# Kernel optimization log

Measured on AMD Instinct MI355X. Metric: run time of the kernel, lower is better.

## Reference

```python
import jax, jax.numpy as jnp
import numpy as np

# Neighbor offsets (di, dj) such that shifted[i, j] = x[i + di, j + dj],
# matching the original ZeroPad2d+slice construction for gates 1..8:
# (left-top, center-top, right-top, left-center, right-center,
#  left-bottom, center-bottom, right-bottom)
OFFSETS = ((1, 1), (1, 0), (1, -1), (0, 1), (0, -1), (-1, 1), (-1, 0), (-1, -1))
PROP_TIME = 4


def _shift(x, di, dj):
    """Zero-padded spatial shift over the last two dims: out[i,j] = x[i+di, j+dj]."""
    xp = jnp.pad(x, [(0, 0)] * (x.ndim - 2) + [(1, 1), (1, 1)])
    H, W = x.shape[-2], x.shape[-1]
    return xp[..., 1 + di:1 + di + H, 1 + dj:1 + dj + W]


def setup_inputs() -> dict:
    key = jax.random.key(0)
    k1, k2 = jax.random.split(key)
    guidance = jax.random.normal(k1, (16, 8, 512, 512), dtype=jnp.float32)
    blur_depth = jax.random.normal(k2, (16, 1, 512, 512), dtype=jnp.float32)
    return {"guidance": guidance, "blur_depth": blur_depth}


def reference(guidance, blur_depth):
    # guidance: [B, 8, H, W]; blur_depth: [B, C=1, H, W]
    # Shifted gates: equivalent to pad-by-offset then slice [1:-1, 1:-1].
    gate_wb = jnp.stack(
        [_shift(guidance[:, k], di, dj) for k, (di, dj) in enumerate(OFFSETS)],
        axis=1,
    )  # [B, 8, H, W]
    abs_weight = jnp.sum(jnp.abs(gate_wb), axis=1, keepdims=True)  # [B, 1, H, W]
    gate_wb = gate_wb / abs_weight
    gate_sum = jnp.sum(gate_wb, axis=1)  # [B, H, W]

    raw = blur_depth
    result = blur_depth  # [B, C, H, W]
    for _ in range(PROP_TIME):
        shifted = jnp.stack(
            [_shift(result, di, dj) for (di, dj) in OFFSETS], axis=1
        )  # [B, 8, C, H, W]
        # gate_wb broadcast over channel dim C (gate_wb[:, :, None] -> [B,8,1,H,W])
        result = jnp.sum(gate_wb[:, :, None] * shifted, axis=1)  # [B, C, H, W]
        result = (1.0 - gate_sum)[:, None] * raw + result
    return result
```

## Files before the change

### kernel.cpp

```cpp
#include <hip/hip_runtime.h>


#define TILE 32
#define G    40
#define GM   38
#define NTHREADS 512

__launch_bounds__(NTHREADS)
__global__ void affprop_kernel(const float* __restrict__ guidance,
                               const float* __restrict__ blur,
                               float* __restrict__ out) {
    __shared__ float sGate[8][GM * GM];
    __shared__ float sBase[GM * GM];
    __shared__ float sA[G * G];
    __shared__ float sB[G * G];

    const int tid = threadIdx.x;
    const int bx0 = blockIdx.x * TILE;
    const int by0 = blockIdx.y * TILE;
    const int b   = blockIdx.z;

    const long plane = 512L * 512L;
    const float* __restrict__ blurB = blur + (long)b * plane;
    const float* __restrict__ guidB = guidance + (long)b * 8 * plane;
    float* __restrict__ outB = out + (long)b * plane;

    for (int i = tid; i < G * G; i += NTHREADS) {
        int y = i / G, x = i % G;
        int gy = by0 - 4 + y, gx = bx0 - 4 + x;
        float v = 0.f;
        if ((unsigned)gy < 512u && (unsigned)gx < 512u)
            v = blurB[gy * 512 + gx];
        sA[i] = v;
    }
    __syncthreads();

    for (int i = tid; i < GM * GM; i += NTHREADS) {
        int y = i / GM + 1, x = i % GM + 1;
        int gy = by0 - 4 + y, gx = bx0 - 4 + x;
        if ((unsigned)gy < 512u && (unsigned)gx < 512u) {
            const int di[8] = {1, 1, 1, 0, 0, -1, -1, -1};
            const int dj[8] = {1, 0, -1, 1, -1, 1, 0, -1};
            float g[8];
            float aw = 0.f;
            #pragma unroll
            for (int k = 0; k < 8; ++k) {
                int yy = gy + di[k], xx = gx + dj[k];
                float v = 0.f;
                if ((unsigned)yy < 512u && (unsigned)xx < 512u)
                    v = guidB[k * plane + yy * 512 + xx];
                g[k] = v;
                aw += fabsf(v);
            }
            float r = (aw > 0.f) ? (1.0f / aw) : 0.f;
            float gs = 0.f;
            #pragma unroll
            for (int k = 0; k < 8; ++k) {
                float w = g[k] * r;
                sGate[k][i] = w;
                gs += w;
            }
            sBase[i] = (1.0f - gs) * sA[y * G + x];
        } else {
            #pragma unroll
            for (int k = 0; k < 8; ++k) sGate[k][i] = 0.f;
            sBase[i] = 0.f;
        }
    }
    __syncthreads();

    float* src = sA;
    float* dst = sB;
    #pragma unroll
    for (int t = 1; t <= 4; ++t) {
        const int m = t;
        const int w = G - 2 * m;
        const int n = w * w;
        for (int i = tid; i < n; i += NTHREADS) {
            int y = i / w + m, x = i % w + m;
            int gi = (y - 1) * GM + (x - 1);
            float acc = sBase[gi];
            acc += sGate[0][gi] * src[(y + 1) * G + (x + 1)];
            acc += sGate[1][gi] * src[(y + 1) * G + (x    )];
            acc += sGate[2][gi] * src[(y + 1) * G + (x - 1)];
            acc += sGate[3][gi] * src[(y    ) * G + (x + 1)];
            acc += sGate[4][gi] * src[(y    ) * G + (x - 1)];
            acc += sGate[5][gi] * src[(y - 1) * G + (x + 1)];
            acc += sGate[6][gi] * src[(y - 1) * G + (x    )];
            acc += sGate[7][gi] * src[(y - 1) * G + (x - 1)];
            dst[y * G + x] = acc;
        }
        __syncthreads();
        float* tmp = src; src = dst; dst = tmp;
    }

    for (int i = tid; i < TILE * TILE; i += NTHREADS) {
        int y = i / TILE + 4, x = i % TILE + 4;
        int gy = by0 - 4 + y, gx = bx0 - 4 + x;
        outB[gy * 512 + gx] = src[y * G + x];
    }
}

extern "C" void kernel_launch(void* const* d_in, const int* in_sizes, int n_in,
                              void* d_out, int out_size, void* d_ws, size_t ws_size,
                              hipStream_t stream) {
    const float* guidance = (const float*)d_in[0];
    const float* blur     = (const float*)d_in[1];
    float* out            = (float*)d_out;

    dim3 grid(512 / TILE, 512 / TILE, 16);
    affprop_kernel<<<grid, NTHREADS, 0, stream>>>(guidance, blur, out);
}
```

Baseline: 239.6 us.

## Keep per-point gate weights in registers instead of shared memory

Each thread now owns up to three fixed points of the 38x38 gate region and holds their eight normalized gate weights and base term in registers across all four propagation steps, instead of staging them in shared memory. Per-step membership is precomputed as a bitmask, and one barrier plus the shared-memory gate arrays are dropped. This cuts shared-memory footprint (allowing more blocks per CU) and LDS reads per step, at the cost of roughly 30 extra VGPRs per thread and some idle lanes on the shrinking inner regions.

```diff
diff --git a/kernel.cpp b/kernel.cpp
--- a/kernel.cpp
+++ b/kernel.cpp
@@ -4,14 +4,14 @@
 #define TILE 32
 #define G    40
 #define GM   38
+#define NPTS (GM * GM)
 #define NTHREADS 512
+#define PPT 3
 
 __launch_bounds__(NTHREADS)
 __global__ void affprop_kernel(const float* __restrict__ guidance,
                                const float* __restrict__ blur,
                                float* __restrict__ out) {
-    __shared__ float sGate[8][GM * GM];
-    __shared__ float sBase[GM * GM];
     __shared__ float sA[G * G];
     __shared__ float sB[G * G];
 
@@ -35,60 +35,77 @@
     }
     __syncthreads();
 
-    for (int i = tid; i < GM * GM; i += NTHREADS) {
-        int y = i / GM + 1, x = i % GM + 1;
-        int gy = by0 - 4 + y, gx = bx0 - 4 + x;
-        if ((unsigned)gy < 512u && (unsigned)gx < 512u) {
-            const int di[8] = {1, 1, 1, 0, 0, -1, -1, -1};
-            const int dj[8] = {1, 0, -1, 1, -1, 1, 0, -1};
-            float g[8];
-            float aw = 0.f;
+    float ga[PPT][8];
+    float gbase[PPT];
+    int   gaddr[PPT];
+    int   gmsk[PPT];
+
+    const int di[8] = {1, 1, 1, 0, 0, -1, -1, -1};
+    const int dj[8] = {1, 0, -1, 1, -1, 1, 0, -1};
+
+    #pragma unroll
+    for (int p = 0; p < PPT; ++p) {
+        #pragma unroll
+        for (int k = 0; k < 8; ++k) ga[p][k] = 0.f;
+        gbase[p] = 0.f;
+        gaddr[p] = 0;
+        gmsk[p]  = 0;
+
+        int i = tid + p * NTHREADS;
+        if (i < NPTS) {
+            int y = i / GM + 1, x = i % GM + 1;
+            gaddr[p] = (y - 1) * G + (x - 1);
+            int m = 0;
             #pragma unroll
-            for (int k = 0; k < 8; ++k) {
-                int yy = gy + di[k], xx = gx + dj[k];
-                float v = 0.f;
-                if ((unsigned)yy < 512u && (unsigned)xx < 512u)
-                    v = guidB[k * plane + yy * 512 + xx];
-                g[k] = v;
-                aw += fabsf(v);
+            for (int t = 1; t <= 4; ++t)
+                if (y >= t && y < G - t && x >= t && x < G - t) m |= 1 << (t - 1);
+            gmsk[p] = m;
+
+            int gy = by0 - 4 + y, gx = bx0 - 4 + x;
+            if ((unsigned)gy < 512u && (unsigned)gx < 512u) {
+                float g[8];
+                float aw = 0.f;
+                #pragma unroll
+                for (int k = 0; k < 8; ++k) {
+                    int yy = gy + di[k], xx = gx + dj[k];
+                    float v = 0.f;
+                    if ((unsigned)yy < 512u && (unsigned)xx < 512u)
+                        v = guidB[k * plane + yy * 512 + xx];
+                    g[k] = v;
+                    aw += fabsf(v);
+                }
+                float r = (aw > 0.f) ? (1.0f / aw) : 0.f;
+                float gs = 0.f;
+                #pragma unroll
+                for (int k = 0; k < 8; ++k) {
+                    float wv = g[k] * r;
+                    ga[p][k] = wv;
+                    gs += wv;
+                }
+                gbase[p] = (1.0f - gs) * sA[y * G + x];
             }
-            float r = (aw > 0.f) ? (1.0f / aw) : 0.f;
-            float gs = 0.f;
-            #pragma unroll
-            for (int k = 0; k < 8; ++k) {
-                float w = g[k] * r;
-                sGate[k][i] = w;
-                gs += w;
-            }
-            sBase[i] = (1.0f - gs) * sA[y * G + x];
-        } else {
-            #pragma unroll
-            for (int k = 0; k < 8; ++k) sGate[k][i] = 0.f;
-            sBase[i] = 0.f;
         }
     }
-    __syncthreads();
 
     float* src = sA;
     float* dst = sB;
     #pragma unroll
     for (int t = 1; t <= 4; ++t) {
-        const int m = t;
-        const int w = G - 2 * m;
-        const int n = w * w;
-        for (int i = tid; i < n; i += NTHREADS) {
-            int y = i / w + m, x = i % w + m;
-            int gi = (y - 1) * GM + (x - 1);
-            float acc = sBase[gi];
-            acc += sGate[0][gi] * src[(y + 1) * G + (x + 1)];
-            acc += sGate[1][gi] * src[(y + 1) * G + (x    )];
-            acc += sGate[2][gi] * src[(y + 1) * G + (x - 1)];
-            acc += sGate[3][gi] * src[(y    ) * G + (x + 1)];
-            acc += sGate[4][gi] * src[(y    ) * G + (x - 1)];
-            acc += sGate[5][gi] * src[(y - 1) * G + (x + 1)];
-            acc += sGate[6][gi] * src[(y - 1) * G + (x    )];
-            acc += sGate[7][gi] * src[(y - 1) * G + (x - 1)];
-            dst[y * G + x] = acc;
+        #pragma unroll
+        for (int p = 0; p < PPT; ++p) {
+            if (gmsk[p] & (1 << (t - 1))) {
+                const float* s = src + gaddr[p];
+                float acc = gbase[p];
+                acc += ga[p][7] * s[0];
+                acc += ga[p][6] * s[1];
+                acc += ga[p][5] * s[2];
+                acc += ga[p][4] * s[G];
+                acc += ga[p][3] * s[G + 2];
+                acc += ga[p][2] * s[2 * G];
+                acc += ga[p][1] * s[2 * G + 1];
+                acc += ga[p][0] * s[2 * G + 2];
+                dst[gaddr[p] + (G + 1)] = acc;
+            }
         }
         __syncthreads();
         float* tmp = src; src = dst; dst = tmp;
@@ -96,8 +113,7 @@
 
     for (int i = tid; i < TILE * TILE; i += NTHREADS) {
         int y = i / TILE + 4, x = i % TILE + 4;
-        int gy = by0 - 4 + y, gx = bx0 - 4 + x;
-        outB[gy * 512 + gx] = src[y * G + x];
+        outB[(by0 - 4 + y) * 512 + (bx0 - 4 + x)] = src[y * G + x];
     }
 }
 
```

Measured after the change: 218.4 us. -8.8%, faster.

## Keep normalized gates in registers with 64x64 tiles and float4 strip stencils

Applied to the files above, without the earlier changes.

Grows the tile from 32 to 64 with a 72x72 halo and 1024 threads, which shrinks the halo recompute overhead. Each thread now owns 4-wide horizontal strips (up to two slots). It computes the normalized gate weights and base term once into registers instead of shared memory. The four propagation steps read neighbours with float4 shared loads and write float4 results. Interior tiles take a branch-free fast path for the guidance loads, and the reciprocal uses the hardware rcp. Costs are heavy register pressure (about 80 floats per thread) that may limit occupancy, and propagation now runs over the full strip region every step instead of a shrinking window.

```diff
diff --git a/kernel.cpp b/kernel.cpp
--- a/kernel.cpp
+++ b/kernel.cpp
@@ -1,103 +1,175 @@
 #include <hip/hip_runtime.h>
 
 
-#define TILE 32
-#define G    40
-#define GM   38
-#define NTHREADS 512
+#define TILE 64
+#define G    72
+#define GG   (G * G)
+#define NT   1024
+#define SW   18
+#define NROW 70
+#define NSTRIP (SW * NROW)
+#define NSLOT 2
 
-__launch_bounds__(NTHREADS)
+__launch_bounds__(NT)
 __global__ void affprop_kernel(const float* __restrict__ guidance,
                                const float* __restrict__ blur,
                                float* __restrict__ out) {
-    __shared__ float sGate[8][GM * GM];
-    __shared__ float sBase[GM * GM];
-    __shared__ float sA[G * G];
-    __shared__ float sB[G * G];
+    __shared__ float sAbuf[GG + 8];
+    __shared__ float sBbuf[GG + 8];
+    float* sA = sAbuf + 4;
+    float* sB = sBbuf + 4;
 
     const int tid = threadIdx.x;
     const int bx0 = blockIdx.x * TILE;
     const int by0 = blockIdx.y * TILE;
     const int b   = blockIdx.z;
 
-    const long plane = 512L * 512L;
+    const int plane = 512 * 512;
     const float* __restrict__ blurB = blur + (long)b * plane;
     const float* __restrict__ guidB = guidance + (long)b * 8 * plane;
     float* __restrict__ outB = out + (long)b * plane;
 
-    for (int i = tid; i < G * G; i += NTHREADS) {
-        int y = i / G, x = i % G;
+    for (int i = tid; i < GG; i += NT) {
+        int y = i / G, x = i - y * G;
         int gy = by0 - 4 + y, gx = bx0 - 4 + x;
         float v = 0.f;
         if ((unsigned)gy < 512u && (unsigned)gx < 512u)
             v = blurB[gy * 512 + gx];
         sA[i] = v;
     }
-    __syncthreads();
-
-    for (int i = tid; i < GM * GM; i += NTHREADS) {
-        int y = i / GM + 1, x = i % GM + 1;
-        int gy = by0 - 4 + y, gx = bx0 - 4 + x;
-        if ((unsigned)gy < 512u && (unsigned)gx < 512u) {
-            const int di[8] = {1, 1, 1, 0, 0, -1, -1, -1};
-            const int dj[8] = {1, 0, -1, 1, -1, 1, 0, -1};
-            float g[8];
-            float aw = 0.f;
-            #pragma unroll
-            for (int k = 0; k < 8; ++k) {
-                int yy = gy + di[k], xx = gx + dj[k];
-                float v = 0.f;
-                if ((unsigned)yy < 512u && (unsigned)xx < 512u)
-                    v = guidB[k * plane + yy * 512 + xx];
-                g[k] = v;
-                aw += fabsf(v);
-            }
-            float r = (aw > 0.f) ? (1.0f / aw) : 0.f;
-            float gs = 0.f;
-            #pragma unroll
-            for (int k = 0; k < 8; ++k) {
-                float w = g[k] * r;
-                sGate[k][i] = w;
-                gs += w;
-            }
-            sBase[i] = (1.0f - gs) * sA[y * G + x];
-        } else {
-            #pragma unroll
-            for (int k = 0; k < 8; ++k) sGate[k][i] = 0.f;
-            sBase[i] = 0.f;
-        }
+    if (tid < G) { sB[tid] = 0.f; sB[(G - 1) * G + tid] = 0.f; }
+    if (tid < 4) {
+        sAbuf[tid] = 0.f; sAbuf[GG + 4 + tid] = 0.f;
+        sBbuf[tid] = 0.f; sBbuf[GG + 4 + tid] = 0.f;
     }
     __syncthreads();
 
-    float* src = sA;
-    float* dst = sB;
+    float ga[NSLOT][8][4];
+    float gb[NSLOT][4];
+    int   gaddr[NSLOT];
+
+    const int di[8] = {1, 1, 1, 0, 0, -1, -1, -1};
+    const int dj[8] = {1, 0, -1, 1, -1, 1, 0, -1};
+
+    const bool interior = (by0 >= 5) && (by0 <= 443) && (bx0 >= 5) && (bx0 <= 443);
+
     #pragma unroll
-    for (int t = 1; t <= 4; ++t) {
-        const int m = t;
-        const int w = G - 2 * m;
-        const int n = w * w;
-        for (int i = tid; i < n; i += NTHREADS) {
-            int y = i / w + m, x = i % w + m;
-            int gi = (y - 1) * GM + (x - 1);
-            float acc = sBase[gi];
-            acc += sGate[0][gi] * src[(y + 1) * G + (x + 1)];
-            acc += sGate[1][gi] * src[(y + 1) * G + (x    )];
-            acc += sGate[2][gi] * src[(y + 1) * G + (x - 1)];
-            acc += sGate[3][gi] * src[(y    ) * G + (x + 1)];
-            acc += sGate[4][gi] * src[(y    ) * G + (x - 1)];
-            acc += sGate[5][gi] * src[(y - 1) * G + (x + 1)];
-            acc += sGate[6][gi] * src[(y - 1) * G + (x    )];
-            acc += sGate[7][gi] * src[(y - 1) * G + (x - 1)];
-            dst[y * G + x] = acc;
+    for (int p = 0; p < NSLOT; ++p) {
+        int s = tid + p * NT;
+        bool act = (p == 0) || (s < NSTRIP);
+        if (act) {
+            int row = s / SW;
+            int c   = s - row * SW;
+            int y   = row + 1;
+            int x0  = c * 4;
+            int ga_ = y * G + x0;
+            gaddr[p] = ga_;
+
+            int gy  = by0 - 4 + y;
+            int gx0 = bx0 - 4 + x0;
+            float raw[4];
+            { float4 r4 = *(const float4*)&sA[ga_];
+              raw[0] = r4.x; raw[1] = r4.y; raw[2] = r4.z; raw[3] = r4.w; }
+
+            if (interior) {
+                float aw[4] = {0.f, 0.f, 0.f, 0.f};
+                #pragma unroll
+                for (int k = 0; k < 8; ++k) {
+                    const float* gk = guidB + k * plane;
+                    int off = (gy + di[k]) * 512 + gx0 + dj[k];
+                    #pragma unroll
+                    for (int j = 0; j < 4; ++j) {
+                        float v = gk[off + j];
+                        ga[p][k][j] = v;
+                        aw[j] += fabsf(v);
+                    }
+                }
+                #pragma unroll
+                for (int j = 0; j < 4; ++j) {
+                    float r = (aw[j] > 0.f) ? __builtin_amdgcn_rcpf(aw[j]) : 0.f;
+                    float gs = 0.f;
+                    #pragma unroll
+                    for (int k = 0; k < 8; ++k) {
+                        float w = ga[p][k][j] * r;
+                        ga[p][k][j] = w;
+                        gs += w;
+                    }
+                    gb[p][j] = (1.0f - gs) * raw[j];
+                }
+            } else {
+                #pragma unroll
+                for (int j = 0; j < 4; ++j) {
+                    int gx = gx0 + j;
+                    bool vp = ((unsigned)gy < 512u) && ((unsigned)gx < 512u);
+                    float aw = 0.f;
+                    float g[8];
+                    #pragma unroll
+                    for (int k = 0; k < 8; ++k) {
+                        int yy = gy + di[k], xx = gx + dj[k];
+                        bool vn = vp && ((unsigned)yy < 512u) && ((unsigned)xx < 512u);
+                        int cy = min(max(yy, 0), 511);
+                        int cx = min(max(xx, 0), 511);
+                        float v = guidB[k * plane + cy * 512 + cx];
+                        v = vn ? v : 0.f;
+                        g[k] = v;
+                        aw += fabsf(v);
+                    }
+                    float r = (aw > 0.f) ? __builtin_amdgcn_rcpf(aw) : 0.f;
+                    float gs = 0.f;
+                    #pragma unroll
+                    for (int k = 0; k < 8; ++k) {
+                        float w = g[k] * r;
+                        ga[p][k][j] = w;
+                        gs += w;
+                    }
+                    gb[p][j] = (1.0f - gs) * raw[j];
+                }
+            }
         }
-        __syncthreads();
-        float* tmp = src; src = dst; dst = tmp;
     }
 
-    for (int i = tid; i < TILE * TILE; i += NTHREADS) {
-        int y = i / TILE + 4, x = i % TILE + 4;
-        int gy = by0 - 4 + y, gx = bx0 - 4 + x;
-        outB[gy * 512 + gx] = src[y * G + x];
+    auto prop = [&](const float* __restrict__ src, float* __restrict__ dst) {
+        #pragma unroll
+        for (int p = 0; p < NSLOT; ++p) {
+            if (p == 0 || tid < (NSTRIP - NT)) {
+                const float* s = src + gaddr[p];
+                float4 up4 = *(const float4*)(s - G);
+                float4 md4 = *(const float4*)(s);
+                float4 dn4 = *(const float4*)(s + G);
+                float u[6] = { s[-G - 1], up4.x, up4.y, up4.z, up4.w, s[-G + 4] };
+                float m[6] = { s[-1],     md4.x, md4.y, md4.z, md4.w, s[4]      };
+                float d[6] = { s[G - 1],  dn4.x, dn4.y, dn4.z, dn4.w, s[G + 4]  };
+                float o[4];
+                #pragma unroll
+                for (int j = 0; j < 4; ++j) {
+                    float acc = gb[p][j];
+                    acc += ga[p][0][j] * d[j + 2];
+                    acc += ga[p][1][j] * d[j + 1];
+                    acc += ga[p][2][j] * d[j];
+                    acc += ga[p][3][j] * m[j + 2];
+                    acc += ga[p][4][j] * m[j];
+                    acc += ga[p][5][j] * u[j + 2];
+                    acc += ga[p][6][j] * u[j + 1];
+                    acc += ga[p][7][j] * u[j];
+                    o[j] = acc;
+                }
+                float4 o4; o4.x = o[0]; o4.y = o[1]; o4.z = o[2]; o4.w = o[3];
+                *(float4*)(dst + gaddr[p]) = o4;
+            }
+        }
+    };
+
+    prop(sA, sB); __syncthreads();
+    prop(sB, sA); __syncthreads();
+    prop(sA, sB); __syncthreads();
+    prop(sB, sA); __syncthreads();
+
+    {
+        int i  = tid;
+        int yy = (i >> 4) + 4;
+        int xx = ((i & 15) << 2) + 4;
+        float4 v = *(const float4*)&sA[yy * G + xx];
+        *(float4*)&outB[(by0 - 4 + yy) * 512 + (bx0 - 4 + xx)] = v;
     }
 }
 
@@ -107,7 +179,8 @@
     const float* guidance = (const float*)d_in[0];
     const float* blur     = (const float*)d_in[1];
     float* out            = (float*)d_out;
+    (void)d_ws; (void)ws_size;
 
     dim3 grid(512 / TILE, 512 / TILE, 16);
-    affprop_kernel<<<grid, NTHREADS, 0, stream>>>(guidance, blur, out);
+    affprop_kernel<<<grid, NT, 0, stream>>>(guidance, blur, out);
 }
```

Measured after the change: 245.2 us. 1.02x slower.
